# Optimization experiments

Measured on AMD Instinct MI355X. Metric: run time of the kernel, lower is better.

## Reference

```python
import jax, jax.numpy as jnp
import numpy as np

B, S, H = 2, 2048, 2048
NH = 16
Q_LORA, KV_LORA = 1536, 512
D_NOPE, D_ROPE, D_V = 128, 64, 128
D_QK = D_NOPE + D_ROPE
SCALE = 1.0 / np.sqrt(D_QK)
EPS = 1e-6


def _freqs(seq_len):
    # precompute_freqs_cis with scaling_factor=1.0 -> plain RoPE
    inv = 1.0 / (10000.0 ** (np.arange(0, D_ROPE, 2, dtype=np.float32) / D_ROPE))
    t = np.arange(seq_len, dtype=np.float32)
    f = np.outer(t, inv)  # (S, D_ROPE//2)
    return jnp.asarray(np.cos(f)), jnp.asarray(np.sin(f))


def _rope_interleaved(x, cos, sin):
    # x: (B, S, heads, D_ROPE); cos/sin: (S, D_ROPE//2)
    b, s, h, d = x.shape
    xr = x.reshape(b, s, h, d // 2, 2)
    e, o = xr[..., 0], xr[..., 1]
    c = cos[None, :, None, :]
    sn = sin[None, :, None, :]
    re = e * c - o * sn
    im = e * sn + o * c
    return jnp.stack([re, im], axis=-1).reshape(b, s, h, d)


def _rmsnorm(x, w):
    xf = x.astype(jnp.float32)
    rms = jnp.sqrt(jnp.mean(xf * xf, axis=-1, keepdims=True) + EPS)
    return (w * (xf / rms)).astype(x.dtype)


def setup_inputs() -> dict:
    key = jax.random.key(0)
    ks = jax.random.split(key, 6)
    def w(k, shape, fan_in):
        return jax.random.normal(k, shape, dtype=jnp.float32) * (1.0 / np.sqrt(fan_in))
    return {
        "hidden_states": jax.random.normal(ks[0], (B, S, H), dtype=jnp.float32),
        "wq_a": w(ks[1], (Q_LORA, H), H),
        "q_norm_w": jnp.ones((Q_LORA,), dtype=jnp.float32),
        "wq_b": w(ks[2], (NH * D_QK, Q_LORA), Q_LORA),
        "wkv_a": w(ks[3], (KV_LORA + D_ROPE, H), H),
        "kv_norm_w": jnp.ones((KV_LORA,), dtype=jnp.float32),
        "wkv_b": w(ks[4], (NH * (D_NOPE + D_V), KV_LORA), KV_LORA),
        "wo": w(ks[5], (H, NH * D_V), NH * D_V),
    }


def reference(hidden_states, wq_a, q_norm_w, wq_b, wkv_a, kv_norm_w, wkv_b, wo):
    b, s, _ = hidden_states.shape
    cos, sin = _freqs(s)

    # low-rank Q path
    q = hidden_states @ wq_a.T                      # (B,S,Q_LORA)
    q = _rmsnorm(q, q_norm_w)
    q = (q @ wq_b.T).reshape(b, s, NH, D_QK)        # (B,S,NH,192)
    q_nope, q_pe = q[..., :D_NOPE], q[..., D_NOPE:]

    # joint KV compression
    kv = hidden_states @ wkv_a.T                    # (B,S,KV_LORA+D_ROPE)
    kv_c, k_pe = kv[..., :KV_LORA], kv[..., KV_LORA:]
    kv_c = _rmsnorm(kv_c, kv_norm_w)
    k_pe = _rope_interleaved(k_pe[:, :, None, :], cos, sin)  # (B,S,1,64)

    kv_x = (kv_c @ wkv_b.T).reshape(b, s, NH, D_NOPE + D_V)
    k_nope, v = kv_x[..., :D_NOPE], kv_x[..., D_NOPE:]

    q_pe = _rope_interleaved(q_pe, cos, sin)
    qf = jnp.concatenate([q_nope, q_pe], axis=-1)   # (B,S,NH,192)
    kf = jnp.concatenate([k_nope, jnp.broadcast_to(k_pe, (b, s, NH, D_ROPE))], axis=-1)

    scores = jnp.einsum("bqhd,bkhd->bhqk", qf, kf) * SCALE
    attn = jax.nn.softmax(scores.astype(jnp.float32), axis=-1).astype(qf.dtype)
    out = jnp.einsum("bhqk,bkhd->bqhd", attn, v).reshape(b, s, NH * D_V)
    return out @ wo.T
```

## Files before the change

### kernel.cpp

```cpp
#include <hip/hip_runtime.h>
#include <math.h>

#define B_   2
#define S_   2048
#define H_   2048
#define NH_  16
#define T_   (B_*S_)
#define QL   1536
#define KVL  512
#define DN   128
#define DR   64
#define DQK  192
#define DV   128
#define SCALE_ 0.07216878364870323f
#define EPS_ 1e-6f

typedef unsigned short u16;
typedef __attribute__((ext_vector_type(8))) short bf16x8;
typedef __attribute__((ext_vector_type(4))) float f32x4;

__device__ __forceinline__ u16 f2b(float x) {
  union { float f; unsigned u; } v; v.f = x;
  unsigned r = v.u + 0x7FFFu + ((v.u >> 16) & 1u);
  return (u16)(r >> 16);
}
__device__ __forceinline__ float b2f(u16 u) {
  union { unsigned u; float f; } v; v.u = ((unsigned)u) << 16; return v.f;
}

#define GLD16(src, dst) __builtin_amdgcn_global_load_lds(                       \
    (const __attribute__((address_space(1))) unsigned int*)(src),               \
    (__attribute__((address_space(3))) unsigned int*)(dst), 16, 0, 0)

__device__ __forceinline__ void cvt4(const float* in, u16* out, int i) {
  float4 v = ((const float4*)in)[i];
  u16 r[4] = {f2b(v.x), f2b(v.y), f2b(v.z), f2b(v.w)};
  ((uint2*)out)[i] = *(uint2*)r;
}

__global__ __launch_bounds__(256) void cvt_all(
    const float* __restrict__ hid, const float* __restrict__ wqa,
    const float* __restrict__ wqb, const float* __restrict__ wkva,
    const float* __restrict__ wkvb, const float* __restrict__ wo,
    u16* __restrict__ o_hid, u16* __restrict__ o_wqa, u16* __restrict__ o_wqb,
    u16* __restrict__ o_wkva, u16* __restrict__ o_wkvb, u16* __restrict__ o_wo) {
  int i = blockIdx.x * 256 + threadIdx.x;
  if (i < 2097152) { cvt4(hid, o_hid, i); return; }
  i -= 2097152;
  if (i < 786432) { cvt4(wqa, o_wqa, i); return; }
  i -= 786432;
  if (i < 1179648) { cvt4(wqb, o_wqb, i); return; }
  i -= 1179648;
  if (i < 327680) {
    int row = i >> 9;
    u16 r[4] = {0, 0, 0, 0};
    if (row < 576) {
      float4 v = ((const float4*)wkva)[i];
      r[0] = f2b(v.x); r[1] = f2b(v.y); r[2] = f2b(v.z); r[3] = f2b(v.w);
    }
    ((uint2*)o_wkva)[i] = *(uint2*)r;
    return;
  }
  i -= 327680;
  if (i < 524288) { cvt4(wkvb, o_wkvb, i); return; }
  i -= 524288;
  if (i < 1048576) cvt4(wo, o_wo, i);
}

template <int OUTMODE>
__global__ __launch_bounds__(256) void gemm_mfma(
    const u16* __restrict__ A, int lda,
    const u16* __restrict__ W, int ldw,
    float* __restrict__ Cf, u16* __restrict__ Cb, int ldc,
    int K, float outscale) {
  __shared__ u16 As[4096];
  __shared__ u16 Bs[4096];
  const int tid = threadIdx.x;
  const int wave = tid >> 6, lane = tid & 63, quad = lane >> 4, l16 = lane & 15;
  const int wm = (wave >> 1) * 64, wn = (wave & 1) * 64;
  const size_t m0 = (size_t)blockIdx.y * 128, n0 = (size_t)blockIdx.x * 128;

  f32x4 acc[4][4];
#pragma unroll
  for (int i = 0; i < 4; ++i)
#pragma unroll
    for (int j = 0; j < 4; ++j) acc[i][j] = (f32x4){0.f, 0.f, 0.f, 0.f};

  const int g0 = tid, g1 = tid + 256;
  const u16* a0 = A + (m0 + (g0 >> 6) * 16 + (g0 & 15)) * (size_t)lda + ((g0 >> 4) & 3) * 8;
  const u16* a1 = A + (m0 + (g1 >> 6) * 16 + (g1 & 15)) * (size_t)lda + ((g1 >> 4) & 3) * 8;
  const u16* b0 = W + (n0 + (g0 >> 6) * 16 + (g0 & 15)) * (size_t)ldw + ((g0 >> 4) & 3) * 8;
  const u16* b1 = W + (n0 + (g1 >> 6) * 16 + (g1 & 15)) * (size_t)ldw + ((g1 >> 4) & 3) * 8;

  for (int k0 = 0; k0 < K; k0 += 32) {
    __syncthreads();
    GLD16(a0 + k0, &As[g0 * 8]);
    GLD16(a1 + k0, &As[g1 * 8]);
    GLD16(b0 + k0, &Bs[g0 * 8]);
    GLD16(b1 + k0, &Bs[g1 * 8]);
    __syncthreads();

    bf16x8 af[4], bfr[4];
#pragma unroll
    for (int i = 0; i < 4; ++i)
      af[i] = *(const bf16x8*)&As[((wm >> 4) + i) * 512 + quad * 128 + l16 * 8];
#pragma unroll
    for (int j = 0; j < 4; ++j)
      bfr[j] = *(const bf16x8*)&Bs[((wn >> 4) + j) * 512 + quad * 128 + l16 * 8];
#pragma unroll
    for (int i = 0; i < 4; ++i)
#pragma unroll
      for (int j = 0; j < 4; ++j)
        acc[i][j] = __builtin_amdgcn_mfma_f32_16x16x32_bf16(af[i], bfr[j], acc[i][j], 0, 0, 0);
  }

#pragma unroll
  for (int i = 0; i < 4; ++i)
#pragma unroll
    for (int j = 0; j < 4; ++j)
#pragma unroll
      for (int r = 0; r < 4; ++r) {
        size_t m = m0 + wm + i * 16 + quad * 4 + r;
        size_t n = n0 + wn + j * 16 + l16;
        if (OUTMODE == 0) Cf[m * ldc + n] = acc[i][j][r];
        else              Cb[m * ldc + n] = f2b(acc[i][j][r] * outscale);
      }
}

__global__ __launch_bounds__(256) void rmsnorm_bf(
    const float* __restrict__ x, const float* __restrict__ w,
    u16* __restrict__ o, int D, int sx, int so) {
  const float* p = x + (size_t)blockIdx.x * sx;
  u16* q = o + (size_t)blockIdx.x * so;
  float ss = 0.f;
  for (int i = threadIdx.x; i < D; i += 256) { float v = p[i]; ss += v * v; }
#pragma unroll
  for (int off = 32; off; off >>= 1) ss += __shfl_down(ss, off);
  __shared__ float red[4];
  __shared__ float s_inv;
  if ((threadIdx.x & 63) == 0) red[threadIdx.x >> 6] = ss;
  __syncthreads();
  if (threadIdx.x == 0) {
    float t = red[0] + red[1] + red[2] + red[3];
    s_inv = 1.0f / sqrtf(t / (float)D + EPS_);
  }
  __syncthreads();
  float inv = s_inv;
  for (int i = threadIdx.x; i < D; i += 256) q[i] = f2b(w[i] * p[i] * inv);
}

__global__ void rope_q_bf(u16* __restrict__ Q) {
  int idx = blockIdx.x * blockDim.x + threadIdx.x;
  int pair = idx & 31;
  int head = (idx >> 5) & (NH_ - 1);
  int row = idx >> 9;
  if (row >= T_) return;
  int s = row & (S_ - 1);
  float inv = powf(10000.0f, -(float)(2 * pair) * (1.0f / 64.0f));
  float ang = (float)s * inv;
  float c = cosf(ang), sn = sinf(ang);
  u16* p = Q + (size_t)row * (NH_ * DQK) + head * DQK + DN + 2 * pair;
  unsigned u = *(unsigned*)p;
  float e = b2f((u16)(u & 0xffff)), o = b2f((u16)(u >> 16));
  float re = e * c - o * sn;
  float im = e * sn + o * c;
  *(unsigned*)p = (unsigned)f2b(re) | ((unsigned)f2b(im) << 16);
}

__global__ void kpe_bf_kernel(const float* __restrict__ KVa, u16* __restrict__ KPE) {
  int idx = blockIdx.x * blockDim.x + threadIdx.x;
  int pair = idx & 31;
  int row = idx >> 5;
  if (row >= T_) return;
  int s = row & (S_ - 1);
  float inv = powf(10000.0f, -(float)(2 * pair) * (1.0f / 64.0f));
  float ang = (float)s * inv;
  float c = cosf(ang), sn = sinf(ang);
  const float* p = KVa + (size_t)row * 640 + KVL + 2 * pair;
  float e = p[0], o = p[1];
  float re = e * c - o * sn;
  float im = e * sn + o * c;
  *(unsigned*)(KPE + (size_t)row * 64 + 2 * pair) =
      (unsigned)f2b(re) | ((unsigned)f2b(im) << 16);
}

__global__ __launch_bounds__(256) void conv_vt(const u16* __restrict__ KVbf,
                                               u16* __restrict__ Vt) {
  const int h = blockIdx.y, b = blockIdx.z;
  const int s0 = (blockIdx.x >> 1) * 64, d0 = (blockIdx.x & 1) * 64;
  const int t0 = b * S_;
  __shared__ u16 tile[64][72];
  const int tid = threadIdx.x;
#pragma unroll
  for (int i = 0; i < 2; ++i) {
    int c = tid + i * 256;
    int row = c >> 3, off = (c & 7) * 8;
    *(uint4*)&tile[row][off] =
        *(const uint4*)(KVbf + (size_t)(t0 + s0 + row) * 4096 + h * 256 + 128 + d0 + off);
  }
  __syncthreads();
#pragma unroll
  for (int i = 0; i < 2; ++i) {
    int c = tid + i * 256;
    int drow = c >> 3, soff = (c & 7) * 8;
    u16 vals[8];
#pragma unroll
    for (int j = 0; j < 8; ++j) vals[j] = tile[soff + j][drow];
    *(uint4*)(Vt + ((size_t)(b * NH_ + h) * 128 + d0 + drow) * 2048 + s0 + soff) =
        *(uint4*)vals;
  }
}

__global__ __launch_bounds__(512, 4) void flash_mfma(
    const u16* __restrict__ Qbf,
    const u16* __restrict__ KVbf,
    const u16* __restrict__ KPE,
    const u16* __restrict__ Vt,
    u16* __restrict__ Out) {
  const int h = blockIdx.y, b = blockIdx.z;
  const int q0 = blockIdx.x * 128;
  const int t0 = b * S_;
  const int tid = threadIdx.x;
  const int wave = tid >> 6, lane = tid & 63, quad = lane >> 4, l16 = lane & 15;

  __shared__ u16 Ks[64 * 192];
  __shared__ u16 Vs[128 * 64];
  u16* Ps = &Ks[wave * 1024];

  bf16x8 qf[6];
  {
    const u16* qp = Qbf + (size_t)(t0 + q0 + wave * 16 + l16) * (NH_ * DQK) + h * DQK + quad * 8;
#pragma unroll
    for (int c = 0; c < 6; ++c) qf[c] = *(const bf16x8*)(qp + c * 32);
  }

  const u16* kbase[3]; int kstep[3];
#pragma unroll
  for (int i = 0; i < 3; ++i) {
    int g = i * 512 + tid;
    int r = g & 15, cc = (g >> 4) % 24, kk = (g >> 4) / 24;
    int tok = kk * 16 + r;
    if (cc < 16) { kbase[i] = KVbf + (size_t)(t0 + tok) * 4096 + h * 256 + cc * 8; kstep[i] = 64 * 4096; }
    else         { kbase[i] = KPE + (size_t)(t0 + tok) * 64 + (cc - 16) * 8;       kstep[i] = 64 * 64; }
  }
  const u16* vbase[2];
#pragma unroll
  for (int i = 0; i < 2; ++i) {
    int g = i * 512 + tid;
    int r = g & 15, kc = (g >> 4) & 7, dt = g >> 7;
    vbase[i] = Vt + ((size_t)((b * NH_ + h) * 128) + dt * 16 + r) * 2048 + kc * 8;
  }

  f32x4 of[8];
#pragma unroll
  for (int i = 0; i < 8; ++i) of[i] = (f32x4){0.f, 0.f, 0.f, 0.f};
  float mrun[4] = {-3e38f, -3e38f, -3e38f, -3e38f};
  float lrun[4] = {0.f, 0.f, 0.f, 0.f};

  for (int kt = 0; kt < S_; kt += 64) {
    __syncthreads();
#pragma unroll
    for (int i = 0; i < 3; ++i) GLD16(kbase[i], &Ks[(i * 512 + tid) * 8]);
#pragma unroll
    for (int i = 0; i < 2; ++i) GLD16(vbase[i] + kt, &Vs[(i * 512 + tid) * 8]);
#pragma unroll
    for (int i = 0; i < 3; ++i) kbase[i] += kstep[i];
    __syncthreads();

    f32x4 sc[4];
#pragma unroll
    for (int kk = 0; kk < 4; ++kk) {
      f32x4 s = (f32x4){0.f, 0.f, 0.f, 0.f};
#pragma unroll
      for (int c = 0; c < 6; ++c) {
        bf16x8 kf = *(const bf16x8*)&Ks[((kk * 24 + c * 4 + quad) * 16 + l16) * 8];
        s = __builtin_amdgcn_mfma_f32_16x16x32_bf16(qf[c], kf, s, 0, 0, 0);
      }
      sc[kk] = s;
    }

    float tm[4], rs[4], alpha[4];
#pragma unroll
    for (int r = 0; r < 4; ++r)
      tm[r] = fmaxf(fmaxf(sc[0][r], sc[1][r]), fmaxf(sc[2][r], sc[3][r]));
#pragma unroll
    for (int off = 1; off < 16; off <<= 1)
#pragma unroll
      for (int r = 0; r < 4; ++r) tm[r] = fmaxf(tm[r], __shfl_xor(tm[r], off, 64));
#pragma unroll
    for (int r = 0; r < 4; ++r) {
      float mnew = fmaxf(mrun[r], tm[r]);
      alpha[r] = __expf(mrun[r] - mnew);
      mrun[r] = mnew;
      float s0 = 0.f;
#pragma unroll
      for (int kk = 0; kk < 4; ++kk) {
        float pv = __expf(sc[kk][r] - mnew);
        sc[kk][r] = pv;
        s0 += pv;
      }
      rs[r] = s0;
    }
#pragma unroll
    for (int off = 1; off < 16; off <<= 1)
#pragma unroll
      for (int r = 0; r < 4; ++r) rs[r] += __shfl_xor(rs[r], off, 64);
#pragma unroll
    for (int r = 0; r < 4; ++r) lrun[r] = lrun[r] * alpha[r] + rs[r];

    __syncthreads();

#pragma unroll
    for (int kk = 0; kk < 4; ++kk)
#pragma unroll
      for (int r = 0; r < 4; ++r)
        Ps[((kk * 2 + (l16 >> 3)) * 16 + quad * 4 + r) * 8 + (l16 & 7)] = f2b(sc[kk][r]);

#pragma unroll
    for (int dt = 0; dt < 8; ++dt)
#pragma unroll
      for (int r = 0; r < 4; ++r) of[dt][r] *= alpha[r];

    bf16x8 pa[2];
#pragma unroll
    for (int c2 = 0; c2 < 2; ++c2)
      pa[c2] = *(const bf16x8*)&Ps[((c2 * 4 + quad) * 16 + l16) * 8];
#pragma unroll
    for (int dt = 0; dt < 8; ++dt) {
#pragma unroll
      for (int c2 = 0; c2 < 2; ++c2) {
        bf16x8 vf = *(const bf16x8*)&Vs[((dt * 8 + c2 * 4 + quad) * 16 + l16) * 8];
        of[dt] = __builtin_amdgcn_mfma_f32_16x16x32_bf16(pa[c2], vf, of[dt], 0, 0, 0);
      }
    }
  }

#pragma unroll
  for (int r = 0; r < 4; ++r) {
    float inv = 1.0f / lrun[r];
    u16* op = Out + (size_t)(t0 + q0 + wave * 16 + quad * 4 + r) * (NH_ * DV) + h * DV + l16;
#pragma unroll
    for (int dt = 0; dt < 8; ++dt) op[dt * 16] = f2b(of[dt][r] * inv);
  }
}

extern "C" void kernel_launch(void* const* d_in, const int* in_sizes, int n_in,
                              void* d_out, int out_size, void* d_ws, size_t ws_size,
                              hipStream_t stream) {
  const float* hidden  = (const float*)d_in[0];
  const float* wq_a    = (const float*)d_in[1];
  const float* q_norm  = (const float*)d_in[2];
  const float* wq_b    = (const float*)d_in[3];
  const float* wkv_a   = (const float*)d_in[4];
  const float* kv_norm = (const float*)d_in[5];
  const float* wkv_b   = (const float*)d_in[6];
  const float* wo      = (const float*)d_in[7];
  float* out = (float*)d_out;

  float* ws = (float*)d_ws;
  u16*   hid_bf  = (u16*)(ws);
  u16*   wqa_bf  = (u16*)(ws + 4194304);
  u16*   wqb_bf  = (u16*)(ws + 5767168);
  u16*   wkva_bf = (u16*)(ws + 8126464);
  u16*   wkvb_bf = (u16*)(ws + 8781824);
  u16*   wo_bf   = (u16*)(ws + 9830400);
  float* q_a     = ws + 11927552;
  u16*   attn_bf = (u16*)(ws + 11927552);
  u16*   qn_bf   = (u16*)(ws + 18219008);
  u16*   vt      = (u16*)(ws + 18219008);
  float* kv_a    = ws + 19791872;
  u16*   q_bf    = (u16*)(ws + 22413312);
  u16*   kvn_bf  = (u16*)(ws + 28704768);
  u16*   kpe     = (u16*)(ws + 29753344);
  u16*   kv_bf   = (u16*)(ws + 29884416);
  const size_t need = (size_t)38273024 * sizeof(float);
  if (ws_size < need) return;

  cvt_all<<<23296, 256, 0, stream>>>(hidden, wq_a, wq_b, wkv_a, wkv_b, wo,
                                     hid_bf, wqa_bf, wqb_bf, wkva_bf, wkvb_bf, wo_bf);

  gemm_mfma<0><<<dim3(QL / 128, T_ / 128), 256, 0, stream>>>(
      hid_bf, H_, wqa_bf, H_, q_a, nullptr, QL, H_, 1.0f);
  rmsnorm_bf<<<T_, 256, 0, stream>>>(q_a, q_norm, qn_bf, QL, QL, QL);
  gemm_mfma<1><<<dim3(NH_ * DQK / 128, T_ / 128), 256, 0, stream>>>(
      qn_bf, QL, wqb_bf, QL, nullptr, q_bf, NH_ * DQK, QL, SCALE_);
  rope_q_bf<<<T_ * NH_ * 32 / 256, 256, 0, stream>>>(q_bf);

  gemm_mfma<0><<<dim3(640 / 128, T_ / 128), 256, 0, stream>>>(
      hid_bf, H_, wkva_bf, H_, kv_a, nullptr, 640, H_, 1.0f);
  rmsnorm_bf<<<T_, 256, 0, stream>>>(kv_a, kv_norm, kvn_bf, KVL, 640, KVL);
  kpe_bf_kernel<<<T_ * 32 / 256, 256, 0, stream>>>(kv_a, kpe);
  gemm_mfma<1><<<dim3(NH_ * (DN + DV) / 128, T_ / 128), 256, 0, stream>>>(
      kvn_bf, KVL, wkvb_bf, KVL, nullptr, kv_bf, NH_ * (DN + DV), KVL, 1.0f);
  conv_vt<<<dim3(64, NH_, B_), 256, 0, stream>>>(kv_bf, vt);

  flash_mfma<<<dim3(S_ / 128, NH_, B_), 512, 0, stream>>>(q_bf, kv_bf, kpe, vt, attn_bf);

  gemm_mfma<0><<<dim3(H_ / 128, T_ / 128), 256, 0, stream>>>(
      attn_bf, NH_ * DV, wo_bf, NH_ * DV, out, nullptr, H_, NH_ * DV, 1.0f);
}
```

Baseline: 653.4 us.

## Double-buffer K/V tiles and keep softmax probabilities in registers via transposed MFMA

The flash attention loop now uses two LDS buffers for K and V. The next tile's global-to-LDS load is issued before computing on the current tile, which removes one barrier per iteration. The MFMA operands are swapped so each lane holds a single query row: the softmax max and sum need only two cross-lane shuffles, and the P tile is rearranged with register shuffles instead of an LDS round trip. Output stores become 8-byte vectorized writes. LDS use doubles, which may lower occupancy below the requested four blocks per CU.

Result: faster. 611.4 us (-6.4%).

```diff
diff --git a/kernel.cpp b/kernel.cpp
--- a/kernel.cpp
+++ b/kernel.cpp
@@ -223,9 +223,8 @@
   const int tid = threadIdx.x;
   const int wave = tid >> 6, lane = tid & 63, quad = lane >> 4, l16 = lane & 15;
 
-  __shared__ u16 Ks[64 * 192];
-  __shared__ u16 Vs[128 * 64];
-  u16* Ps = &Ks[wave * 1024];
+  __shared__ u16 Ks[2][64 * 192];
+  __shared__ u16 Vs[2][128 * 64];
 
   bf16x8 qf[6];
   {
@@ -254,18 +253,27 @@
   f32x4 of[8];
 #pragma unroll
   for (int i = 0; i < 8; ++i) of[i] = (f32x4){0.f, 0.f, 0.f, 0.f};
-  float mrun[4] = {-3e38f, -3e38f, -3e38f, -3e38f};
-  float lrun[4] = {0.f, 0.f, 0.f, 0.f};
-
-  for (int kt = 0; kt < S_; kt += 64) {
+  float mrun = -3e38f, lrun = 0.f;
+
+#pragma unroll
+  for (int i = 0; i < 3; ++i) { GLD16(kbase[i], &Ks[0][(i * 512 + tid) * 8]); kbase[i] += kstep[i]; }
+#pragma unroll
+  for (int i = 0; i < 2; ++i) GLD16(vbase[i], &Vs[0][(i * 512 + tid) * 8]);
+
+  const int src_lo = (quad & 1) * 32 + l16;
+  const int src_hi = src_lo + 16;
+  const bool hi_kk = (quad >> 1) != 0;
+
+  for (int it = 0; it < S_ / 64; ++it) {
+    const int cur = it & 1;
     __syncthreads();
-#pragma unroll
-    for (int i = 0; i < 3; ++i) GLD16(kbase[i], &Ks[(i * 512 + tid) * 8]);
-#pragma unroll
-    for (int i = 0; i < 2; ++i) GLD16(vbase[i] + kt, &Vs[(i * 512 + tid) * 8]);
-#pragma unroll
-    for (int i = 0; i < 3; ++i) kbase[i] += kstep[i];
-    __syncthreads();
+
+    if (it + 1 < S_ / 64) {
+#pragma unroll
+      for (int i = 0; i < 3; ++i) { GLD16(kbase[i], &Ks[cur ^ 1][(i * 512 + tid) * 8]); kbase[i] += kstep[i]; }
+#pragma unroll
+      for (int i = 0; i < 2; ++i) GLD16(vbase[i] + (it + 1) * 64, &Vs[cur ^ 1][(i * 512 + tid) * 8]);
+    }
 
     f32x4 sc[4];
 #pragma unroll
@@ -273,74 +281,80 @@
       f32x4 s = (f32x4){0.f, 0.f, 0.f, 0.f};
 #pragma unroll
       for (int c = 0; c < 6; ++c) {
-        bf16x8 kf = *(const bf16x8*)&Ks[((kk * 24 + c * 4 + quad) * 16 + l16) * 8];
-        s = __builtin_amdgcn_mfma_f32_16x16x32_bf16(qf[c], kf, s, 0, 0, 0);
+        bf16x8 kf = *(const bf16x8*)&Ks[cur][((kk * 24 + c * 4 + quad) * 16 + l16) * 8];
+        s = __builtin_amdgcn_mfma_f32_16x16x32_bf16(kf, qf[c], s, 0, 0, 0);
       }
       sc[kk] = s;
     }
 
-    float tm[4], rs[4], alpha[4];
-#pragma unroll
-    for (int r = 0; r < 4; ++r)
-      tm[r] = fmaxf(fmaxf(sc[0][r], sc[1][r]), fmaxf(sc[2][r], sc[3][r]));
-#pragma unroll
-    for (int off = 1; off < 16; off <<= 1)
-#pragma unroll
-      for (int r = 0; r < 4; ++r) tm[r] = fmaxf(tm[r], __shfl_xor(tm[r], off, 64));
-#pragma unroll
-    for (int r = 0; r < 4; ++r) {
-      float mnew = fmaxf(mrun[r], tm[r]);
-      alpha[r] = __expf(mrun[r] - mnew);
-      mrun[r] = mnew;
-      float s0 = 0.f;
-#pragma unroll
-      for (int kk = 0; kk < 4; ++kk) {
-        float pv = __expf(sc[kk][r] - mnew);
-        sc[kk][r] = pv;
-        s0 += pv;
+    float tm = sc[0][0];
+#pragma unroll
+    for (int kk = 0; kk < 4; ++kk)
+#pragma unroll
+      for (int r = 0; r < 4; ++r) tm = fmaxf(tm, sc[kk][r]);
+    tm = fmaxf(tm, __shfl_xor(tm, 16, 64));
+    tm = fmaxf(tm, __shfl_xor(tm, 32, 64));
+    float mnew = fmaxf(mrun, tm);
+    float alpha = __expf(mrun - mnew);
+    mrun = mnew;
+    float lsum = 0.f;
+#pragma unroll
+    for (int kk = 0; kk < 4; ++kk)
+#pragma unroll
+      for (int r = 0; r < 4; ++r) {
+        float p = __expf(sc[kk][r] - mnew);
+        sc[kk][r] = p;
+        lsum += p;
       }
-      rs[r] = s0;
-    }
-#pragma unroll
-    for (int off = 1; off < 16; off <<= 1)
-#pragma unroll
-      for (int r = 0; r < 4; ++r) rs[r] += __shfl_xor(rs[r], off, 64);
-#pragma unroll
-    for (int r = 0; r < 4; ++r) lrun[r] = lrun[r] * alpha[r] + rs[r];
-
-    __syncthreads();
-
-#pragma unroll
-    for (int kk = 0; kk < 4; ++kk)
-#pragma unroll
-      for (int r = 0; r < 4; ++r)
-        Ps[((kk * 2 + (l16 >> 3)) * 16 + quad * 4 + r) * 8 + (l16 & 7)] = f2b(sc[kk][r]);
-
-#pragma unroll
-    for (int dt = 0; dt < 8; ++dt)
-#pragma unroll
-      for (int r = 0; r < 4; ++r) of[dt][r] *= alpha[r];
+    lsum += __shfl_xor(lsum, 16, 64);
+    lsum += __shfl_xor(lsum, 32, 64);
+    lrun = lrun * alpha + lsum;
+
+    unsigned pb[4][2];
+#pragma unroll
+    for (int kk = 0; kk < 4; ++kk) {
+      pb[kk][0] = (unsigned)f2b(sc[kk][0]) | ((unsigned)f2b(sc[kk][1]) << 16);
+      pb[kk][1] = (unsigned)f2b(sc[kk][2]) | ((unsigned)f2b(sc[kk][3]) << 16);
+    }
 
     bf16x8 pa[2];
 #pragma unroll
-    for (int c2 = 0; c2 < 2; ++c2)
-      pa[c2] = *(const bf16x8*)&Ps[((c2 * 4 + quad) * 16 + l16) * 8];
+    for (int c2 = 0; c2 < 2; ++c2) {
+      unsigned a0 = __shfl(pb[c2 * 2][0], src_lo, 64);
+      unsigned b0 = __shfl(pb[c2 * 2 + 1][0], src_lo, 64);
+      unsigned a1 = __shfl(pb[c2 * 2][1], src_lo, 64);
+      unsigned b1 = __shfl(pb[c2 * 2 + 1][1], src_lo, 64);
+      unsigned a2 = __shfl(pb[c2 * 2][0], src_hi, 64);
+      unsigned b2 = __shfl(pb[c2 * 2 + 1][0], src_hi, 64);
+      unsigned a3 = __shfl(pb[c2 * 2][1], src_hi, 64);
+      unsigned b3 = __shfl(pb[c2 * 2 + 1][1], src_hi, 64);
+      union { unsigned w[4]; bf16x8 v; } u;
+      u.w[0] = hi_kk ? b0 : a0;
+      u.w[1] = hi_kk ? b1 : a1;
+      u.w[2] = hi_kk ? b2 : a2;
+      u.w[3] = hi_kk ? b3 : a3;
+      pa[c2] = u.v;
+    }
+
 #pragma unroll
     for (int dt = 0; dt < 8; ++dt) {
 #pragma unroll
+      for (int r = 0; r < 4; ++r) of[dt][r] *= alpha;
+#pragma unroll
       for (int c2 = 0; c2 < 2; ++c2) {
-        bf16x8 vf = *(const bf16x8*)&Vs[((dt * 8 + c2 * 4 + quad) * 16 + l16) * 8];
-        of[dt] = __builtin_amdgcn_mfma_f32_16x16x32_bf16(pa[c2], vf, of[dt], 0, 0, 0);
+        bf16x8 vf = *(const bf16x8*)&Vs[cur][((dt * 8 + c2 * 4 + quad) * 16 + l16) * 8];
+        of[dt] = __builtin_amdgcn_mfma_f32_16x16x32_bf16(vf, pa[c2], of[dt], 0, 0, 0);
       }
     }
   }
 
-#pragma unroll
-  for (int r = 0; r < 4; ++r) {
-    float inv = 1.0f / lrun[r];
-    u16* op = Out + (size_t)(t0 + q0 + wave * 16 + quad * 4 + r) * (NH_ * DV) + h * DV + l16;
-#pragma unroll
-    for (int dt = 0; dt < 8; ++dt) op[dt * 16] = f2b(of[dt][r] * inv);
+  float inv = 1.0f / lrun;
+  u16* op = Out + (size_t)(t0 + q0 + wave * 16 + l16) * (NH_ * DV) + h * DV + quad * 4;
+#pragma unroll
+  for (int dt = 0; dt < 8; ++dt) {
+    u16 r4[4] = {f2b(of[dt][0] * inv), f2b(of[dt][1] * inv),
+                 f2b(of[dt][2] * inv), f2b(of[dt][3] * inv)};
+    *(uint2*)(op + dt * 16) = *(uint2*)r4;
   }
 }
 
```
